# Optimization experiments

Measured on AMD Instinct MI355X. Metric: run time of the kernel, lower is better.

## Reference

```python
import jax, jax.numpy as jnp
import numpy as np

CHUNK = 512  # tile size along N; keeps per-step [B,CHUNK,M] tile ~64 MB, never builds full [B,N,M]


def setup_inputs() -> dict:
    key = jax.random.key(0)
    k1, k2 = jax.random.split(key)
    xyz1 = jax.random.normal(k1, (4, 8192, 3), dtype=jnp.float32)
    xyz2 = jax.random.normal(k2, (4, 8192, 3), dtype=jnp.float32)
    return {"xyz1": xyz1, "xyz2": xyz2}


def _chamfer(xyz1, xyz2):
    # xyz1: [B,N,3], xyz2: [B,M,3]
    B, N, _ = xyz1.shape
    M = xyz2.shape[1]
    K = N // CHUNK
    x1_chunks = xyz1.reshape(B, K, CHUNK, 3).transpose(1, 0, 2, 3)  # [K,B,C,3]

    def step(carry, x1k):
        best_d2, best_i2, start = carry  # running mins for xyz2 -> xyz1 direction
        # squared distances for this tile: [B,C,M]
        d = jnp.sum((x1k[:, :, None, :] - xyz2[:, None, :, :]) ** 2, axis=-1)
        # xyz1 -> xyz2: min over M
        d1 = jnp.min(d, axis=2)                              # [B,C]
        i1 = jnp.argmin(d, axis=2).astype(jnp.int32)         # [B,C]
        # xyz2 -> xyz1: partial min over this chunk of N
        dc = jnp.min(d, axis=1)                              # [B,M]
        ic = jnp.argmin(d, axis=1).astype(jnp.int32) + start # [B,M], global index
        upd = dc < best_d2
        best_d2 = jnp.where(upd, dc, best_d2)
        best_i2 = jnp.where(upd, ic, best_i2)
        return (best_d2, best_i2, start + CHUNK), (d1, i1)

    init = (jnp.full((B, M), jnp.inf, dtype=xyz1.dtype),
            jnp.zeros((B, M), dtype=jnp.int32),
            jnp.int32(0))
    (dist2, idx2, _), (d1s, i1s) = jax.lax.scan(step, init, x1_chunks)
    dist1 = d1s.transpose(1, 0, 2).reshape(B, N)
    idx1 = i1s.transpose(1, 0, 2).reshape(B, N)
    return dist1, dist2, idx1, idx2


def reference(xyz1, xyz2):
    # Matches ChamferDistance.forward: (dist1, dist2, idx1, idx2),
    # squared nearest-neighbor distances and int32 argmin indices.
    return _chamfer(xyz1, xyz2)
```

## Files before the change

kernel.cpp:

```cpp
#include <hip/hip_runtime.h>
#include <math.h>


#define QPT 8
#define BLK 256
#define QPB (QPT*BLK)

#define LOADF8(J) do {                                                        \
    f0 = sv4[8*(J)+0]; f1 = sv4[8*(J)+1]; f2 = sv4[8*(J)+2];                  \
    f3 = sv4[8*(J)+3]; f4 = sv4[8*(J)+4]; f5 = sv4[8*(J)+5];                  \
    f6 = sv4[8*(J)+6]; f7 = sv4[8*(J)+7];                                     \
} while (0)

#define EMIN8(AX, AY, AZ, MOUT) do {                                          \
    float d0 = fmaf(AX, f0.x, fmaf(AY, f0.y, fmaf(AZ, f0.z, f0.w)));          \
    float d1 = fmaf(AX, f1.x, fmaf(AY, f1.y, fmaf(AZ, f1.z, f1.w)));          \
    float d2 = fmaf(AX, f2.x, fmaf(AY, f2.y, fmaf(AZ, f2.z, f2.w)));          \
    float d3 = fmaf(AX, f3.x, fmaf(AY, f3.y, fmaf(AZ, f3.z, f3.w)));          \
    float d4 = fmaf(AX, f4.x, fmaf(AY, f4.y, fmaf(AZ, f4.z, f4.w)));          \
    float d5 = fmaf(AX, f5.x, fmaf(AY, f5.y, fmaf(AZ, f5.z, f5.w)));          \
    float d6 = fmaf(AX, f6.x, fmaf(AY, f6.y, fmaf(AZ, f6.z, f6.w)));          \
    float d7 = fmaf(AX, f7.x, fmaf(AY, f7.y, fmaf(AZ, f7.z, f7.w)));          \
    float t0 = fminf(fminf(d0, d1), d2);                                      \
    float t1 = fminf(fminf(d3, d4), d5);                                      \
    float t2 = fminf(fminf(d6, d7), t0);                                      \
    MOUT = fminf(t1, t2);                                                     \
} while (0)

#define DMIN8(QX, QY, QZ, MOUT) do {                                          \
    float dx, dy, dz;                                                         \
    dx = QX - f0.x; dy = QY - f0.y; dz = QZ - f0.z;                           \
    float d0 = fmaf(dx, dx, fmaf(dy, dy, dz * dz));                           \
    dx = QX - f1.x; dy = QY - f1.y; dz = QZ - f1.z;                           \
    float d1 = fmaf(dx, dx, fmaf(dy, dy, dz * dz));                           \
    dx = QX - f2.x; dy = QY - f2.y; dz = QZ - f2.z;                           \
    float d2 = fmaf(dx, dx, fmaf(dy, dy, dz * dz));                           \
    dx = QX - f3.x; dy = QY - f3.y; dz = QZ - f3.z;                           \
    float d3 = fmaf(dx, dx, fmaf(dy, dy, dz * dz));                           \
    dx = QX - f4.x; dy = QY - f4.y; dz = QZ - f4.z;                           \
    float d4 = fmaf(dx, dx, fmaf(dy, dy, dz * dz));                           \
    dx = QX - f5.x; dy = QY - f5.y; dz = QZ - f5.z;                           \
    float d5 = fmaf(dx, dx, fmaf(dy, dy, dz * dz));                           \
    dx = QX - f6.x; dy = QY - f6.y; dz = QZ - f6.z;                           \
    float d6 = fmaf(dx, dx, fmaf(dy, dy, dz * dz));                           \
    dx = QX - f7.x; dy = QY - f7.y; dz = QZ - f7.z;                           \
    float d7 = fmaf(dx, dx, fmaf(dy, dy, dz * dz));                           \
    float t0 = fminf(fminf(d0, d1), d2);                                      \
    float t1 = fminf(fminf(d3, d4), d5);                                      \
    float t2 = fminf(fminf(d6, d7), t0);                                      \
    MOUT = fminf(t1, t2);                                                     \
} while (0)

__global__ __launch_bounds__(256, 4) void chamfer_main(
    const float* __restrict__ xyz1, const float* __restrict__ xyz2,
    unsigned long long* __restrict__ pp,
    int N, int M, int B, int S, int C)
{
    const int dir = blockIdx.z;
    const float* q = dir ? xyz2 : xyz1;
    const float* r = dir ? xyz1 : xyz2;
    const int Nq = dir ? M : N;
    const int Nr = dir ? N : M;
    const int b     = blockIdx.y / S;
    const int split = blockIdx.y % S;
    const int base  = split * C;

    extern __shared__ float s[];
    float4* sv4 = (float4*)s;

    {
        const float* g3 = r + ((size_t)b * Nr + base) * 3;
        for (int t = threadIdx.x; t < C; t += BLK) {
            float gx = g3[3 * t + 0], gy = g3[3 * t + 1], gz = g3[3 * t + 2];
            float rr = fmaf(gz, gz, fmaf(gy, gy, gx * gx));
            float4 f; f.x = gx; f.y = gy; f.z = gz; f.w = rr;
            sv4[t] = f;
        }
    }
    __syncthreads();

    float ax[QPT], ay[QPT], az[QPT];
    bool qvv[QPT];
#pragma unroll
    for (int k = 0; k < QPT; ++k) {
        const int qidx = blockIdx.x * QPB + k * BLK + threadIdx.x;
        qvv[k] = qidx < Nq;
        const float* qp = q + ((size_t)b * Nq + (qvv[k] ? qidx : 0)) * 3;
        ax[k] = -2.0f * qp[0]; ay[k] = -2.0f * qp[1]; az[k] = -2.0f * qp[2];
    }

    float e1[QPT], e2[QPT];
    int   g1[QPT];
#pragma unroll
    for (int k = 0; k < QPT; ++k) { e1[k] = INFINITY; e2[k] = INFINITY; g1[k] = 0; }

    const int iters = C / 8;
    for (int j8 = 0; j8 < iters; ++j8) {
        float4 f0, f1, f2, f3, f4, f5, f6, f7;
        LOADF8(j8);
#pragma unroll
        for (int k = 0; k < QPT; ++k) {
            float m;
            EMIN8(ax[k], ay[k], az[k], m);
            float h = fmaxf(e1[k], m);
            e2[k] = fminf(e2[k], h);
            if (m < e1[k]) g1[k] = j8;
            e1[k] = fminf(e1[k], m);
        }
    }

    const size_t obase = (size_t)(dir * B + b) * Nq;
    const int gbase = split * (C / 8);
#pragma unroll
    for (int k = 0; k < QPT; ++k) {
        if (!qvv[k]) continue;
        const int qidx = blockIdx.x * QPB + k * BLK + threadIdx.x;
        const float qx = -0.5f * ax[k], qy = -0.5f * ay[k], qz = -0.5f * az[k];
        int gi = g1[k];
        float dwin;
        bool resolved = false;
        {
            float qq  = fmaf(qx, qx, fmaf(qy, qy, qz * qz));
            float d1e = qq + e1[k];
            float rt  = sqrtf(qq) + sqrtf(fmaxf(d1e, 0.0f) + 0.01f);
            float eps = 4e-6f * fmaf(2.0f, rt * rt, qq);
            if (e2[k] - e1[k] <= eps) {
                const float lim = e1[k] + eps;
                unsigned long long mask = 0ull;
                for (int j8 = 0; j8 < iters; ++j8) {
                    float4 f0, f1, f2, f3, f4, f5, f6, f7;
                    LOADF8(j8);
                    float m;
                    EMIN8(ax[k], ay[k], az[k], m);
                    if (m <= lim) mask |= 1ull << j8;
                }
                float bdx = INFINITY; int gs = 0;
                for (int j8 = 0; j8 < iters; ++j8) {
                    if (!((mask >> j8) & 1)) continue;
                    float4 f0, f1, f2, f3, f4, f5, f6, f7;
                    LOADF8(j8);
                    float md;
                    DMIN8(qx, qy, qz, md);
                    if (md < bdx) { bdx = md; gs = j8; }
                }
                gi = gs; dwin = bdx; resolved = true;
            }
        }
        if (!resolved) {
            const float4* rv =
                (const float4*)(r + ((size_t)b * Nr + base + (size_t)gi * 8) * 3);
            float4 h0 = rv[0], h1 = rv[1], h2 = rv[2],
                   h3 = rv[3], h4 = rv[4], h5 = rv[5];
            float px[8] = { h0.x, h0.w, h1.z, h2.y, h3.x, h3.w, h4.z, h5.y };
            float py[8] = { h0.y, h1.x, h1.w, h2.z, h3.y, h4.x, h4.w, h5.z };
            float pz[8] = { h0.z, h1.y, h2.x, h2.w, h3.z, h4.y, h5.x, h5.w };
            float d[8];
#pragma unroll
            for (int p = 0; p < 8; ++p) {
                float dx = qx - px[p];
                float dy = qy - py[p];
                float dz = qz - pz[p];
                d[p] = fmaf(dx, dx, fmaf(dy, dy, dz * dz));
            }
            float t0 = fminf(fminf(d[0], d[1]), d[2]);
            float t1 = fminf(fminf(d[3], d[4]), d[5]);
            float t2 = fminf(fminf(d[6], d[7]), t0);
            dwin = fminf(t1, t2);
        }
        unsigned long long packed =
            ((unsigned long long)__float_as_uint(dwin) << 32)
            | (unsigned)(gbase + gi);
        atomicMin(&pp[obase + qidx], packed);
    }
}

__global__ __launch_bounds__(256) void chamfer_final(
    const float* __restrict__ xyz1, const float* __restrict__ xyz2,
    const unsigned long long* __restrict__ pp,
    float* __restrict__ out, int N, int M, int B)
{
    const int gid = blockIdx.x * blockDim.x + threadIdx.x;
    const int perDir0 = B * N;
    int dir, rem;
    if (gid < perDir0) { dir = 0; rem = gid; }
    else if (gid < perDir0 + B * M) { dir = 1; rem = gid - perDir0; }
    else return;
    const int Nq = dir ? M : N;
    const int Nr = dir ? N : M;
    const float* q = dir ? xyz2 : xyz1;
    const float* r = dir ? xyz1 : xyz2;

    unsigned long long v = pp[(size_t)(dir * B) * Nq + rem];
    const unsigned bits = (unsigned)(v >> 32);
    const int grp = (int)(v & 0xffffffffu);

    const int b  = rem / Nq;
    const int qi = rem - b * Nq;
    const float* qp = q + ((size_t)b * Nq + qi) * 3;
    const float qx = qp[0], qy = qp[1], qz = qp[2];

    const float4* rv = (const float4*)(r + ((size_t)b * Nr + (size_t)grp * 8) * 3);
    float4 f0 = rv[0], f1 = rv[1], f2 = rv[2], f3 = rv[3], f4 = rv[4], f5 = rv[5];
    float px[8] = { f0.x, f0.w, f1.z, f2.y, f3.x, f3.w, f4.z, f5.y };
    float py[8] = { f0.y, f1.x, f1.w, f2.z, f3.y, f4.x, f4.w, f5.z };
    float pz[8] = { f0.z, f1.y, f2.x, f2.w, f3.z, f4.y, f5.x, f5.w };
    int best = 0;
#pragma unroll
    for (int p = 7; p >= 0; --p) {
        float dx = qx - px[p];
        float dy = qy - py[p];
        float dz = qz - pz[p];
        float d = fmaf(dx, dx, fmaf(dy, dy, dz * dz));
        if (__float_as_uint(d) == bits) best = p;
    }
    const int idx = grp * 8 + best;

    float* dist_out = out + (dir ? (size_t)B * N : 0);
    float* idx_out  = out + (size_t)B * N + (size_t)B * M + (dir ? (size_t)B * N : 0);
    dist_out[rem] = __uint_as_float(bits);
    idx_out[rem]  = (float)idx;
}

extern "C" void kernel_launch(void* const* d_in, const int* in_sizes, int n_in,
                              void* d_out, int out_size, void* d_ws, size_t ws_size,
                              hipStream_t stream) {
    const float* xyz1 = (const float*)d_in[0];
    const float* xyz2 = (const float*)d_in[1];
    float* out = (float*)d_out;
    const int B = 4;
    const int N = in_sizes[0] / (B * 3);
    const int M = in_sizes[1] / (B * 3);
    const int NQ = (N > M ? N : M);
    const int NR = (N > M ? N : M);

    int S = 32;
    while (NR % (S * 8)) S >>= 1;
    const int C = NR / S;

    unsigned long long* pp = (unsigned long long*)d_ws;
    const int nslots = 2 * B * NQ;

    hipMemsetAsync(pp, 0xFF, (size_t)nslots * 8, stream);

    dim3 grid((NQ + QPB - 1) / QPB, B * S, 2);
    size_t lds = (size_t)C * 4 * sizeof(float);
    chamfer_main<<<grid, dim3(BLK, 1, 1), lds, stream>>>(
        xyz1, xyz2, pp, N, M, B, S, C);

    chamfer_final<<<dim3((nslots + 255) / 256, 1, 1), dim3(256, 1, 1), 0, stream>>>(
        xyz1, xyz2, pp, out, N, M, B);
}
```

Baseline: 120.5 us.

## Fuse finalize pass into main kernel via last-block ticket counter

Removes the separate chamfer_final launch. Each main block increments a per-(dir,batch,query-tile) ticket after its atomicMin updates, and the last-arriving split block finalizes that query slice: it reads the packed min, recomputes the winning index within the group of 8, and writes the outputs. Queries per thread drop from 8 to 4, which doubles the grid and shrinks each finalize slice. The ticket array is zeroed by the same memset (filled with 0xFF, so counting starts at -1, hence the S-2 test). This saves one launch and its pass over the workspace, but adds a threadfence plus a serialized tail of work in the last blocks.

```diff
diff --git a/kernel.cpp b/kernel.cpp
--- a/kernel.cpp
+++ b/kernel.cpp
@@ -2,7 +2,7 @@
 #include <math.h>
 
 
-#define QPT 8
+#define QPT 4
 #define BLK 256
 #define QPB (QPT*BLK)
 
@@ -51,9 +51,50 @@
     MOUT = fminf(t1, t2);                                                     \
 } while (0)
 
+__device__ __noinline__ void finalize_slice(
+    const float* __restrict__ q, const float* __restrict__ r,
+    unsigned long long* __restrict__ pp, float* __restrict__ out,
+    int dir, int b, int Nq, int Nr, int N, int M, int B, int qstart)
+{
+    const size_t obase = (size_t)(dir * B + b) * Nq;
+    float* dist_out = out + (dir ? (size_t)B * N : 0) + (size_t)b * Nq;
+    float* idx_out  = out + (size_t)B * N + (size_t)B * M
+                          + (dir ? (size_t)B * N : 0) + (size_t)b * Nq;
+    for (int t = threadIdx.x; t < QPB; t += BLK) {
+        const int qidx = qstart + t;
+        if (qidx >= Nq) break;
+        unsigned long long v = atomicMin(&pp[obase + qidx], ~0ull);
+        const unsigned bits = (unsigned)(v >> 32);
+        const int grp = (int)(v & 0xffffffffu);
+
+        const float* qp = q + ((size_t)b * Nq + qidx) * 3;
+        const float qx = qp[0], qy = qp[1], qz = qp[2];
+
+        const float4* rv =
+            (const float4*)(r + ((size_t)b * Nr + (size_t)grp * 8) * 3);
+        float4 f0 = rv[0], f1 = rv[1], f2 = rv[2],
+               f3 = rv[3], f4 = rv[4], f5 = rv[5];
+        float px[8] = { f0.x, f0.w, f1.z, f2.y, f3.x, f3.w, f4.z, f5.y };
+        float py[8] = { f0.y, f1.x, f1.w, f2.z, f3.y, f4.x, f4.w, f5.z };
+        float pz[8] = { f0.z, f1.y, f2.x, f2.w, f3.z, f4.y, f5.x, f5.w };
+        int best = 0;
+#pragma unroll
+        for (int p = 7; p >= 0; --p) {
+            float dx = qx - px[p];
+            float dy = qy - py[p];
+            float dz = qz - pz[p];
+            float d = fmaf(dx, dx, fmaf(dy, dy, dz * dz));
+            if (__float_as_uint(d) == bits) best = p;
+        }
+        dist_out[qidx] = __uint_as_float(bits);
+        idx_out[qidx]  = (float)(grp * 8 + best);
+    }
+}
+
 __global__ __launch_bounds__(256, 4) void chamfer_main(
     const float* __restrict__ xyz1, const float* __restrict__ xyz2,
-    unsigned long long* __restrict__ pp,
+    unsigned long long* __restrict__ pp, unsigned* __restrict__ tick,
+    float* __restrict__ out,
     int N, int M, int B, int S, int C)
 {
     const int dir = blockIdx.z;
@@ -172,53 +213,21 @@
             | (unsigned)(gbase + gi);
         atomicMin(&pp[obase + qidx], packed);
     }
-}
-
-__global__ __launch_bounds__(256) void chamfer_final(
-    const float* __restrict__ xyz1, const float* __restrict__ xyz2,
-    const unsigned long long* __restrict__ pp,
-    float* __restrict__ out, int N, int M, int B)
-{
-    const int gid = blockIdx.x * blockDim.x + threadIdx.x;
-    const int perDir0 = B * N;
-    int dir, rem;
-    if (gid < perDir0) { dir = 0; rem = gid; }
-    else if (gid < perDir0 + B * M) { dir = 1; rem = gid - perDir0; }
-    else return;
-    const int Nq = dir ? M : N;
-    const int Nr = dir ? N : M;
-    const float* q = dir ? xyz2 : xyz1;
-    const float* r = dir ? xyz1 : xyz2;
-
-    unsigned long long v = pp[(size_t)(dir * B) * Nq + rem];
-    const unsigned bits = (unsigned)(v >> 32);
-    const int grp = (int)(v & 0xffffffffu);
-
-    const int b  = rem / Nq;
-    const int qi = rem - b * Nq;
-    const float* qp = q + ((size_t)b * Nq + qi) * 3;
-    const float qx = qp[0], qy = qp[1], qz = qp[2];
-
-    const float4* rv = (const float4*)(r + ((size_t)b * Nr + (size_t)grp * 8) * 3);
-    float4 f0 = rv[0], f1 = rv[1], f2 = rv[2], f3 = rv[3], f4 = rv[4], f5 = rv[5];
-    float px[8] = { f0.x, f0.w, f1.z, f2.y, f3.x, f3.w, f4.z, f5.y };
-    float py[8] = { f0.y, f1.x, f1.w, f2.z, f3.y, f4.x, f4.w, f5.z };
-    float pz[8] = { f0.z, f1.y, f2.x, f2.w, f3.z, f4.y, f5.x, f5.w };
-    int best = 0;
-#pragma unroll
-    for (int p = 7; p >= 0; --p) {
-        float dx = qx - px[p];
-        float dy = qy - py[p];
-        float dz = qz - pz[p];
-        float d = fmaf(dx, dx, fmaf(dy, dy, dz * dz));
-        if (__float_as_uint(d) == bits) best = p;
-    }
-    const int idx = grp * 8 + best;
-
-    float* dist_out = out + (dir ? (size_t)B * N : 0);
-    float* idx_out  = out + (size_t)B * N + (size_t)B * M + (dir ? (size_t)B * N : 0);
-    dist_out[rem] = __uint_as_float(bits);
-    idx_out[rem]  = (float)idx;
+
+    __threadfence();
+    __syncthreads();
+    __shared__ unsigned winflag;
+    if (threadIdx.x == 0) {
+        const unsigned ti = (unsigned)((dir * B + b) * gridDim.x + blockIdx.x);
+        unsigned old = atomicAdd(&tick[ti], 1u);
+        winflag = (old == (unsigned)(S - 2)) ? 1u : 0u;
+    }
+    __syncthreads();
+    if (winflag) {
+        __threadfence();
+        finalize_slice(q, r, pp, out, dir, b, Nq, Nr, N, M, B,
+                       blockIdx.x * QPB);
+    }
 }
 
 extern "C" void kernel_launch(void* const* d_in, const int* in_sizes, int n_in,
@@ -237,16 +246,17 @@
     while (NR % (S * 8)) S >>= 1;
     const int C = NR / S;
 
+    const int X = (NQ + QPB - 1) / QPB;
     unsigned long long* pp = (unsigned long long*)d_ws;
     const int nslots = 2 * B * NQ;
-
-    hipMemsetAsync(pp, 0xFF, (size_t)nslots * 8, stream);
-
-    dim3 grid((NQ + QPB - 1) / QPB, B * S, 2);
+    const size_t ppBytes = (size_t)nslots * 8;
+    unsigned* tick = (unsigned*)((char*)d_ws + ppBytes);
+    const size_t tickBytes = (size_t)2 * B * X * sizeof(unsigned);
+
+    hipMemsetAsync(pp, 0xFF, ppBytes + tickBytes, stream);
+
+    dim3 grid(X, B * S, 2);
     size_t lds = (size_t)C * 4 * sizeof(float);
     chamfer_main<<<grid, dim3(BLK, 1, 1), lds, stream>>>(
-        xyz1, xyz2, pp, N, M, B, S, C);
-
-    chamfer_final<<<dim3((nslots + 255) / 256, 1, 1), dim3(256, 1, 1), 0, stream>>>(
-        xyz1, xyz2, pp, out, N, M, B);
+        xyz1, xyz2, pp, tick, out, N, M, B, S, C);
 }
```

Result: slower. 323.2 us (+168.3%).
